# Performance work log

Measured on AMD Instinct MI355X. Metric: run time of the kernel, lower is better.

## Reference

```python
import jax, jax.numpy as jnp
import numpy as np

N, E, G = 200000, 800000, 8000
NODE_IN, EDGE_IN, H = 256, 64, 256


def _mlp2(h, w1, b1, w2, b2):
    return jax.nn.relu(h @ w1 + b1) @ w2 + b2


def setup_inputs() -> dict:
    key = jax.random.key(0)
    ks = jax.random.split(key, 30)
    s = 0.05
    p = lambda k, shp: (jax.random.normal(k, shp, jnp.float32) * s)
    inp = {
        "x": jax.random.normal(ks[0], (N, NODE_IN), jnp.float32),
        "edge_attr": jax.random.normal(ks[1], (E, EDGE_IN), jnp.float32),
        "edge_index": jax.random.randint(ks[2], (2, E), 0, N, dtype=jnp.int32),
        "batch": jnp.sort(jax.random.randint(ks[3], (N,), 0, G, dtype=jnp.int32)),
        # edge MLP
        "em_w1": p(ks[4], (EDGE_IN, H)), "em_b1": jnp.zeros((H,), jnp.float32),
        "em_w2": p(ks[5], (H, H)), "em_b2": jnp.zeros((H,), jnp.float32),
        # GINEConv 1 MLP
        "c1_w1": p(ks[6], (NODE_IN, H)), "c1_b1": jnp.zeros((H,), jnp.float32),
        "c1_w2": p(ks[7], (H, H)), "c1_b2": jnp.zeros((H,), jnp.float32),
        # GINEConv 2 MLP
        "c2_w1": p(ks[8], (H, H)), "c2_b1": jnp.zeros((H,), jnp.float32),
        "c2_w2": p(ks[9], (H, H)), "c2_b2": jnp.zeros((H,), jnp.float32),
        # heads
        "l1_w": p(ks[10], (H, 128)), "l1_b": jnp.zeros((128,), jnp.float32),
        "l2_w": p(ks[11], (128, 64)), "l2_b": jnp.zeros((64,), jnp.float32),
        "hS_w": p(ks[12], (64, 1)), "hS_b": jnp.zeros((1,), jnp.float32),
        "hP_w": p(ks[13], (64, 1)), "hP_b": jnp.zeros((1,), jnp.float32),
        "hN_w": p(ks[14], (64, 1)), "hN_b": jnp.zeros((1,), jnp.float32),
    }
    return inp


def _gine(x, ea, src, dst, w1, b1, w2, b2):
    # GINEConv (eps=0): out = MLP(x_i + sum_j relu(x_j + e_ji))
    msg = jax.nn.relu(x[src] + ea)                      # [E, H]
    agg = jax.ops.segment_sum(msg, dst, num_segments=x.shape[0])
    return _mlp2(x + agg, w1, b1, w2, b2)


def reference(x, edge_attr, edge_index, batch,
              em_w1, em_b1, em_w2, em_b2,
              c1_w1, c1_b1, c1_w2, c1_b2,
              c2_w1, c2_b1, c2_w2, c2_b2,
              l1_w, l1_b, l2_w, l2_b,
              hS_w, hS_b, hP_w, hP_b, hN_w, hN_b):
    src, dst = edge_index[0], edge_index[1]  # source_to_target flow
    ea = _mlp2(edge_attr, em_w1, em_b1, em_w2, em_b2)   # [E, 256]
    h = jax.nn.relu(_gine(x, ea, src, dst, c1_w1, c1_b1, c1_w2, c1_b2))
    h = jax.nn.relu(_gine(h, ea, src, dst, c2_w1, c2_b1, c2_w2, c2_b2))
    # global mean pool over graphs (dropout is identity in eval mode)
    sums = jax.ops.segment_sum(h, batch, num_segments=G)              # [G, 256]
    cnts = jax.ops.segment_sum(jnp.ones((h.shape[0],), h.dtype), batch, num_segments=G)
    pooled = sums / jnp.maximum(cnts, 1.0)[:, None]
    g = jax.nn.relu(pooled @ l1_w + l1_b)
    g = jax.nn.relu(g @ l2_w + l2_b)
    return ((g @ hS_w + hS_b).squeeze(-1),
            (g @ hP_w + hP_b).squeeze(-1),
            (g @ hN_w + hN_b).squeeze(-1))
```

## Files before the change

kernel.cpp:

```cpp
#include <hip/hip_runtime.h>
#include <hip/hip_bf16.h>

typedef __attribute__((ext_vector_type(8))) short short8;
typedef __attribute__((ext_vector_type(4))) float f32x4;
typedef __attribute__((ext_vector_type(2))) unsigned int u32x2;
typedef __attribute__((ext_vector_type(4))) unsigned int u32x4;

#define N_NODES  200000
#define N_EDGES  800000
#define N_GRAPHS 8000

__device__ __forceinline__ unsigned short f2bf(float f) {
  unsigned int u = __float_as_uint(f);
  unsigned int r = (u + 0x7fffu + ((u >> 16) & 1u)) >> 16;
  return (unsigned short)r;
}
__device__ __forceinline__ float bf2f(unsigned short s) {
  return __uint_as_float(((unsigned int)s) << 16);
}
__device__ __forceinline__ unsigned cvtpk(float a, float b) {
  union { __hip_bfloat162 h; unsigned u; } cv;
  cv.h = __float22bfloat162_rn(make_float2(a, b));
  return cv.u;
}

__device__ __forceinline__ void xpose4(unsigned W0, unsigned W1, int bsub,
                                       unsigned selT, unsigned& T0, unsigned& T1) {
  unsigned t0 = (unsigned)__shfl_xor((int)W0, 2);
  unsigned t1 = (unsigned)__shfl_xor((int)W1, 2);
  unsigned A0 = (bsub & 2) ? t1 : W0;
  unsigned A1 = (bsub & 2) ? W1 : t0;
  unsigned t2 = (unsigned)__shfl_xor((int)A0, 1);
  unsigned t3 = (unsigned)__shfl_xor((int)A1, 1);
  T0 = __builtin_amdgcn_perm(A0, t2, selT);
  T1 = __builtin_amdgcn_perm(A1, t3, selT);
}

__global__ void wtrans(const float* __restrict__ w, unsigned short* __restrict__ wt,
                       int K, int Nc) {
  int id = blockIdx.x * 256 + threadIdx.x;
  if (id >= K * Nc) return;
  int k = id / Nc, n = id % Nc;
  wt[n * K + k] = f2bf(w[id]);
}

__global__ __launch_bounds__(256) void x2bf(const float* __restrict__ x,
                                            unsigned short* __restrict__ xb) {
  int id = blockIdx.x * 256 + threadIdx.x;
  if (id >= N_NODES * 256 / 8) return;
  float4 a = ((const float4*)x)[id * 2];
  float4 b = ((const float4*)x)[id * 2 + 1];
  u32x4 pk = {cvtpk(a.x, a.y), cvtpk(a.z, a.w), cvtpk(b.x, b.y), cvtpk(b.z, b.w)};
  ((u32x4*)xb)[id] = pk;
}

template <int K1, int IN_MODE, int SLAB, int NKK>
__device__ __forceinline__ void stage_slab(
    int s, char* ab, int row0, int srow, int skk,
    const float* __restrict__ Xf, const unsigned short* __restrict__ Xb,
    const unsigned short* __restrict__ aggb) {
#pragma unroll
  for (int c2 = 0; c2 < NKK; ++c2) {
    const int kloc = skk + 32 * c2;
    const int gk = s * SLAB + kloc;
    float v[8];
    if (IN_MODE == 0) {
      const float* xp = Xf + (size_t)(row0 + srow) * K1 + gk;
      float4 A = *(const float4*)xp;
      float4 B = *(const float4*)(xp + 4);
      v[0]=A.x; v[1]=A.y; v[2]=A.z; v[3]=A.w; v[4]=B.x; v[5]=B.y; v[6]=B.z; v[7]=B.w;
    } else {
      const unsigned short* hp = Xb + (size_t)(row0 + srow) * 256 + gk;
      short8 hv = *(const short8*)hp;
      const unsigned short* ap = aggb + (size_t)(row0 + srow) * 256 + gk;
      short8 av = *(const short8*)ap;
#pragma unroll
      for (int i = 0; i < 8; ++i)
        v[i] = bf2f((unsigned short)hv[i]) + bf2f((unsigned short)av[i]);
    }
    u32x4 pk;
#pragma unroll
    for (int i = 0; i < 4; ++i) pk[i] = cvtpk(v[2 * i], v[2 * i + 1]);
    int off = srow * (2 * SLAB) + kloc * 2;
    off ^= (srow & 7) << 4;
    *(u32x4*)(ab + off) = pk;
  }
}

template <int K1, int IN_MODE>
__global__ __launch_bounds__(256) void fused_mlp2(
    const float* __restrict__ Xf, const unsigned short* __restrict__ Xb,
    const unsigned short* __restrict__ aggb,
    const unsigned short* __restrict__ w1t, const float* __restrict__ b1,
    const unsigned short* __restrict__ w2t, const float* __restrict__ b2,
    unsigned short* __restrict__ out, int relu_out) {
  constexpr int SLAB  = (K1 < 128) ? K1 : 128;
  constexpr int NSLAB = K1 / SLAB;
  constexpr int NKK   = SLAB / 32;
  __shared__ unsigned short h_lds[64 * 256];
  char* hbase = (char*)h_lds;

  const int tid  = threadIdx.x;
  const int row0 = blockIdx.x * 64;
  const int lane = tid & 63;
  const int wid  = tid >> 6;
  const int lr   = lane & 15;
  const int kq   = lane >> 4;
  const int col0 = wid * 64;
  const int bsub = lr & 3;
  const int asub = lr >> 2;
  const unsigned selT = (bsub & 1) ? 0x07060302u : 0x01000504u;

  const int srow = tid >> 2;
  const int skk  = (tid & 3) * 8;

  f32x4 acc[4][4];
#pragma unroll
  for (int m = 0; m < 4; ++m)
#pragma unroll
    for (int n = 0; n < 4; ++n) acc[m][n] = (f32x4){0.f, 0.f, 0.f, 0.f};

  float bias1[4];
#pragma unroll
  for (int n = 0; n < 4; ++n) bias1[n] = b1[col0 + n * 16 + lr];

  stage_slab<K1, IN_MODE, SLAB, NKK>(0, hbase, row0, srow, skk, Xf, Xb, aggb);
  __syncthreads();

#pragma unroll
  for (int s = 0; s < NSLAB; ++s) {
    if (s + 1 < NSLAB)
      stage_slab<K1, IN_MODE, SLAB, NKK>(s + 1, hbase + 16384, row0, srow, skk,
                                         Xf, Xb, aggb);
    char* ab = hbase + (s & 1) * 16384;
#pragma unroll
    for (int kk = 0; kk < NKK; ++kk) {
      short8 af[4], bq[4];
#pragma unroll
      for (int m = 0; m < 4; ++m) {
        int r = m * 16 + lr;
        int off = r * (2 * SLAB) + kk * 64 + kq * 16;
        off ^= (r & 7) << 4;
        af[m] = *(short8*)(ab + off);
      }
#pragma unroll
      for (int n = 0; n < 4; ++n) {
        int c = col0 + n * 16 + lr;
        bq[n] = *(const short8*)(w1t + (size_t)c * K1 + s * SLAB + kk * 32 + kq * 8);
      }
#pragma unroll
      for (int m = 0; m < 4; ++m)
#pragma unroll
        for (int n = 0; n < 4; ++n)
          acc[m][n] = __builtin_amdgcn_mfma_f32_16x16x32_bf16(af[m], bq[n], acc[m][n], 0, 0, 0);
    }
    __syncthreads();
  }

#pragma unroll
  for (int n = 0; n < 4; ++n) {
    float bn = bias1[n];
#pragma unroll
    for (int m = 0; m < 4; ++m) {
      float v0 = fmaxf(acc[m][n][0] + bn, 0.f);
      float v1 = fmaxf(acc[m][n][1] + bn, 0.f);
      float v2 = fmaxf(acc[m][n][2] + bn, 0.f);
      float v3 = fmaxf(acc[m][n][3] + bn, 0.f);
      unsigned W0 = cvtpk(v0, v1), W1 = cvtpk(v2, v3), T0, T1;
      xpose4(W0, W1, bsub, selT, T0, T1);
      int r = m * 16 + kq * 4 + bsub;
      int cb = col0 + n * 16 + asub * 4;
      int off = r * 512 + cb * 2;
      off ^= (r & 7) << 4;
      *(u32x2*)(hbase + off) = (u32x2){T0, T1};
    }
  }
  __syncthreads();

#pragma unroll
  for (int m = 0; m < 4; ++m)
#pragma unroll
    for (int n = 0; n < 4; ++n) acc[m][n] = (f32x4){0.f, 0.f, 0.f, 0.f};

  float bias2[4];
#pragma unroll
  for (int n = 0; n < 4; ++n) bias2[n] = b2[col0 + n * 16 + lr];

#pragma unroll
  for (int ks = 0; ks < 8; ++ks) {
    short8 af[4], bq[4];
#pragma unroll
    for (int m = 0; m < 4; ++m) {
      int r = m * 16 + lr;
      int off = r * 512 + ks * 64 + kq * 16;
      off ^= (r & 7) << 4;
      af[m] = *(short8*)(hbase + off);
    }
#pragma unroll
    for (int n = 0; n < 4; ++n) {
      int c = col0 + n * 16 + lr;
      bq[n] = *(const short8*)(w2t + (size_t)c * 256 + ks * 32 + kq * 8);
    }
#pragma unroll
    for (int m = 0; m < 4; ++m)
#pragma unroll
      for (int n = 0; n < 4; ++n)
        acc[m][n] = __builtin_amdgcn_mfma_f32_16x16x32_bf16(af[m], bq[n], acc[m][n], 0, 0, 0);
  }
  __syncthreads();

#pragma unroll
  for (int n = 0; n < 4; ++n) {
    float bn = bias2[n];
#pragma unroll
    for (int m = 0; m < 4; ++m) {
      float v0 = acc[m][n][0] + bn;
      float v1 = acc[m][n][1] + bn;
      float v2 = acc[m][n][2] + bn;
      float v3 = acc[m][n][3] + bn;
      if (relu_out) {
        v0 = fmaxf(v0, 0.f); v1 = fmaxf(v1, 0.f);
        v2 = fmaxf(v2, 0.f); v3 = fmaxf(v3, 0.f);
      }
      unsigned W0 = cvtpk(v0, v1), W1 = cvtpk(v2, v3), T0, T1;
      xpose4(W0, W1, bsub, selT, T0, T1);
      int r = m * 16 + kq * 4 + bsub;
      int cb = col0 + n * 16 + asub * 4;
      int off = r * 512 + cb * 2;
      off ^= (r & 7) << 4;
      *(u32x2*)(hbase + off) = (u32x2){T0, T1};
    }
  }
  __syncthreads();

#pragma unroll
  for (int it = 0; it < 8; ++it) {
    int r = (tid >> 5) + it * 8;
    int byte = (tid & 31) * 16;
    int off = (r * 512 + byte) ^ ((r & 7) << 4);
    u32x4 d = *(u32x4*)(hbase + off);
    *(u32x4*)((char*)out + (size_t)(row0 + r) * 512 + byte) = d;
  }
}

__global__ void hist_deg(const int* __restrict__ dst, int* __restrict__ rp) {
  int e = blockIdx.x * 256 + threadIdx.x;
  if (e < N_EDGES) atomicAdd(&rp[dst[e]], 1);
}

__global__ __launch_bounds__(256) void scan_block(int* __restrict__ rp,
                                                  int* __restrict__ bsum) {
  __shared__ int ts[256];
  int b = blockIdx.x, t = threadIdx.x;
  int base = b * 2048 + t * 8;
  int v[8]; int s = 0;
#pragma unroll
  for (int i = 0; i < 8; ++i) {
    int idx = base + i;
    v[i] = (idx < N_NODES) ? rp[idx] : 0;
    s += v[i];
  }
  ts[t] = s;
  __syncthreads();
#pragma unroll
  for (int off = 1; off < 256; off <<= 1) {
    int add = (t >= off) ? ts[t - off] : 0;
    __syncthreads();
    ts[t] += add;
    __syncthreads();
  }
  int excl = ts[t] - s;
  if (t == 255) bsum[b] = ts[255];
  int run = excl;
#pragma unroll
  for (int i = 0; i < 8; ++i) {
    int idx = base + i;
    if (idx < N_NODES) rp[idx] = run;
    run += v[i];
  }
}

__global__ __launch_bounds__(256) void scan_bsum(int* __restrict__ bsum, int nb) {
  __shared__ int ts[256];
  int t = threadIdx.x;
  int v = (t < nb) ? bsum[t] : 0;
  ts[t] = v;
  __syncthreads();
#pragma unroll
  for (int off = 1; off < 256; off <<= 1) {
    int add = (t >= off) ? ts[t - off] : 0;
    __syncthreads();
    ts[t] += add;
    __syncthreads();
  }
  if (t < nb) bsum[t] = ts[t] - v;
}

__global__ void scan_add(int* __restrict__ rp, const int* __restrict__ bsum) {
  int i = blockIdx.x * 256 + threadIdx.x;
  if (i < N_NODES) rp[i] += bsum[i >> 11];
}

__global__ void csr_fill(const int* __restrict__ src, const int* __restrict__ dst,
                         int* __restrict__ rp, int2* __restrict__ csr) {
  int e = blockIdx.x * 256 + threadIdx.x;
  if (e >= N_EDGES) return;
  int d = dst[e];
  int p = atomicAdd(&rp[d], 1);
  csr[p] = make_int2(src[e], e);
}

__global__ __launch_bounds__(256) void gather_agg(
    const unsigned short* __restrict__ ea, const unsigned short* __restrict__ xb,
    const int* __restrict__ rp, const int2* __restrict__ csr,
    unsigned short* __restrict__ agg) {
  int v = blockIdx.x * 4 + (threadIdx.x >> 6);
  if (v >= N_NODES) return;
  int lane = threadIdx.x & 63;
  int c = lane * 4;
  int beg = (v == 0) ? 0 : rp[v - 1];
  int end = rp[v];
  float a0 = 0.f, a1 = 0.f, a2 = 0.f, a3 = 0.f;
  int i = beg;
  for (; i + 2 <= end; i += 2) {
    int2 s0 = csr[i];
    int2 s1 = csr[i + 1];
    ushort4 e0 = *(const ushort4*)(ea + (size_t)s0.y * 256 + c);
    ushort4 e1 = *(const ushort4*)(ea + (size_t)s1.y * 256 + c);
    ushort4 h0 = *(const ushort4*)(xb + (size_t)s0.x * 256 + c);
    ushort4 h1 = *(const ushort4*)(xb + (size_t)s1.x * 256 + c);
    a0 += fmaxf(bf2f(h0.x) + bf2f(e0.x), 0.f) + fmaxf(bf2f(h1.x) + bf2f(e1.x), 0.f);
    a1 += fmaxf(bf2f(h0.y) + bf2f(e0.y), 0.f) + fmaxf(bf2f(h1.y) + bf2f(e1.y), 0.f);
    a2 += fmaxf(bf2f(h0.z) + bf2f(e0.z), 0.f) + fmaxf(bf2f(h1.z) + bf2f(e1.z), 0.f);
    a3 += fmaxf(bf2f(h0.w) + bf2f(e0.w), 0.f) + fmaxf(bf2f(h1.w) + bf2f(e1.w), 0.f);
  }
  if (i < end) {
    int2 se = csr[i];
    ushort4 ev = *(const ushort4*)(ea + (size_t)se.y * 256 + c);
    ushort4 hv = *(const ushort4*)(xb + (size_t)se.x * 256 + c);
    a0 += fmaxf(bf2f(hv.x) + bf2f(ev.x), 0.f);
    a1 += fmaxf(bf2f(hv.y) + bf2f(ev.y), 0.f);
    a2 += fmaxf(bf2f(hv.z) + bf2f(ev.z), 0.f);
    a3 += fmaxf(bf2f(hv.w) + bf2f(ev.w), 0.f);
  }
  u32x2 pk = {cvtpk(a0, a1), cvtpk(a2, a3)};
  *(u32x2*)(agg + (size_t)v * 256 + c) = pk;
}

__global__ __launch_bounds__(256) void pool_mean(const unsigned short* __restrict__ h2,
                                                 const int* __restrict__ batch,
                                                 float* __restrict__ pooled) {
  int g = blockIdx.x;
  int tid = threadIdx.x;
  int lane = tid & 63;
  int sub = tid >> 6;
  int lo = 0, hi = N_NODES;
  while (lo < hi) { int mid = (lo + hi) >> 1; if (batch[mid] < g) lo = mid + 1; else hi = mid; }
  int start = lo;
  hi = N_NODES;
  while (lo < hi) { int mid = (lo + hi) >> 1; if (batch[mid] < g + 1) lo = mid + 1; else hi = mid; }
  int end = lo;
  float s0 = 0.f, s1 = 0.f, s2 = 0.f, s3 = 0.f;
  for (int r = start + sub; r < end; r += 4) {
    ushort4 hv = *(const ushort4*)(h2 + (size_t)r * 256 + lane * 4);
    s0 += bf2f(hv.x); s1 += bf2f(hv.y); s2 += bf2f(hv.z); s3 += bf2f(hv.w);
  }
  __shared__ float4 red[4][64];
  red[sub][lane] = make_float4(s0, s1, s2, s3);
  __syncthreads();
  if (sub == 0) {
    float4 a = red[0][lane], b = red[1][lane], cc = red[2][lane], d = red[3][lane];
    float inv = 1.0f / fmaxf((float)(end - start), 1.0f);
    float4 t = make_float4((a.x + b.x + cc.x + d.x) * inv,
                           (a.y + b.y + cc.y + d.y) * inv,
                           (a.z + b.z + cc.z + d.z) * inv,
                           (a.w + b.w + cc.w + d.w) * inv);
    *(float4*)(pooled + (size_t)g * 256 + lane * 4) = t;
  }
}

__global__ __launch_bounds__(128) void head_mlp(
    const float* __restrict__ pooled, const float* __restrict__ l1w,
    const float* __restrict__ l1b, const float* __restrict__ l2w,
    const float* __restrict__ l2b, const float* __restrict__ hSw,
    const float* __restrict__ hSb, const float* __restrict__ hPw,
    const float* __restrict__ hPb, const float* __restrict__ hNw,
    const float* __restrict__ hNb, float* __restrict__ out) {
  int g = blockIdx.x, tid = threadIdx.x;
  __shared__ float p[256];
  __shared__ float g1[128];
  __shared__ float g2[64];
  p[tid] = pooled[(size_t)g * 256 + tid];
  p[tid + 128] = pooled[(size_t)g * 256 + tid + 128];
  __syncthreads();
  float a = l1b[tid];
#pragma unroll 8
  for (int k = 0; k < 256; ++k) a += p[k] * l1w[k * 128 + tid];
  g1[tid] = fmaxf(a, 0.f);
  __syncthreads();
  if (tid < 64) {
    float b = l2b[tid];
#pragma unroll 8
    for (int k = 0; k < 128; ++k) b += g1[k] * l2w[k * 64 + tid];
    g2[tid] = fmaxf(b, 0.f);
  }
  __syncthreads();
  if (tid < 64) {
    float v = g2[tid];
    float s = v * hSw[tid], pq = v * hPw[tid], nq = v * hNw[tid];
#pragma unroll
    for (int off = 32; off > 0; off >>= 1) {
      s  += __shfl_down(s, off);
      pq += __shfl_down(pq, off);
      nq += __shfl_down(nq, off);
    }
    if (tid == 0) {
      out[g]                = s  + hSb[0];
      out[N_GRAPHS + g]     = pq + hPb[0];
      out[2 * N_GRAPHS + g] = nq + hNb[0];
    }
  }
}

extern "C" void kernel_launch(void* const* d_in, const int* in_sizes, int n_in,
                              void* d_out, int out_size, void* d_ws, size_t ws_size,
                              hipStream_t stream) {
  const float* x         = (const float*)d_in[0];
  const float* edge_attr = (const float*)d_in[1];
  const int*   ei        = (const int*)d_in[2];
  const int*   batch     = (const int*)d_in[3];
  const float* em_w1 = (const float*)d_in[4];  const float* em_b1 = (const float*)d_in[5];
  const float* em_w2 = (const float*)d_in[6];  const float* em_b2 = (const float*)d_in[7];
  const float* c1_w1 = (const float*)d_in[8];  const float* c1_b1 = (const float*)d_in[9];
  const float* c1_w2 = (const float*)d_in[10]; const float* c1_b2 = (const float*)d_in[11];
  const float* c2_w1 = (const float*)d_in[12]; const float* c2_b1 = (const float*)d_in[13];
  const float* c2_w2 = (const float*)d_in[14]; const float* c2_b2 = (const float*)d_in[15];
  const float* l1_w = (const float*)d_in[16];  const float* l1_b = (const float*)d_in[17];
  const float* l2_w = (const float*)d_in[18];  const float* l2_b = (const float*)d_in[19];
  const float* hS_w = (const float*)d_in[20];  const float* hS_b = (const float*)d_in[21];
  const float* hP_w = (const float*)d_in[22];  const float* hP_b = (const float*)d_in[23];
  const float* hN_w = (const float*)d_in[24];  const float* hN_b = (const float*)d_in[25];

  char* ws = (char*)d_ws;
  unsigned short* ea     = (unsigned short*)ws;
  unsigned short* agg    = (unsigned short*)(ws + 409600000);
  unsigned short* xb     = (unsigned short*)(ws + 512000000);
  unsigned short* h1     = (unsigned short*)(ws + 614400000);
  unsigned short* h2     = ea;
  float*          pooled = (float*)(ws + 716800000);
  int2*           csr    = (int2*)(ws + 716800000);
  int*            rp     = (int*)(ws + 723200000);
  int*            bsum   = (int*)(ws + 724000000);
  unsigned short* wt     = (unsigned short*)(ws + 724992000);
  unsigned short* em_w1t = wt;
  unsigned short* em_w2t = em_w1t + 16384;
  unsigned short* c1_w1t = em_w2t + 65536;
  unsigned short* c1_w2t = c1_w1t + 65536;
  unsigned short* c2_w1t = c1_w2t + 65536;
  unsigned short* c2_w2t = c2_w1t + 65536;

  const int* srcI = ei;
  const int* dstI = ei + N_EDGES;

  wtrans<<<(16384 + 255) / 256, 256, 0, stream>>>(em_w1, em_w1t, 64, 256);
  wtrans<<<(65536 + 255) / 256, 256, 0, stream>>>(em_w2, em_w2t, 256, 256);
  wtrans<<<(65536 + 255) / 256, 256, 0, stream>>>(c1_w1, c1_w1t, 256, 256);
  wtrans<<<(65536 + 255) / 256, 256, 0, stream>>>(c1_w2, c1_w2t, 256, 256);
  wtrans<<<(65536 + 255) / 256, 256, 0, stream>>>(c2_w1, c2_w1t, 256, 256);
  wtrans<<<(65536 + 255) / 256, 256, 0, stream>>>(c2_w2, c2_w2t, 256, 256);

  x2bf<<<(N_NODES * 256 / 8 + 255) / 256, 256, 0, stream>>>(x, xb);

  hipMemsetAsync(rp, 0, (size_t)N_NODES * 4, stream);
  hist_deg<<<(N_EDGES + 255) / 256, 256, 0, stream>>>(dstI, rp);
  scan_block<<<(N_NODES + 2047) / 2048, 256, 0, stream>>>(rp, bsum);
  scan_bsum<<<1, 256, 0, stream>>>(bsum, (N_NODES + 2047) / 2048);
  scan_add<<<(N_NODES + 255) / 256, 256, 0, stream>>>(rp, bsum);
  csr_fill<<<N_EDGES / 256, 256, 0, stream>>>(srcI, dstI, rp, csr);

  fused_mlp2<64, 0><<<N_EDGES / 64, 256, 0, stream>>>(
      edge_attr, nullptr, nullptr, em_w1t, em_b1, em_w2t, em_b2, ea, 0);

  gather_agg<<<(N_NODES + 3) / 4, 256, 0, stream>>>(ea, xb, rp, csr, agg);
  fused_mlp2<256, 2><<<N_NODES / 64, 256, 0, stream>>>(
      nullptr, xb, agg, c1_w1t, c1_b1, c1_w2t, c1_b2, h1, 1);

  gather_agg<<<(N_NODES + 3) / 4, 256, 0, stream>>>(ea, h1, rp, csr, agg);
  fused_mlp2<256, 2><<<N_NODES / 64, 256, 0, stream>>>(
      nullptr, h1, agg, c2_w1t, c2_b1, c2_w2t, c2_b2, h2, 1);

  pool_mean<<<N_GRAPHS, 256, 0, stream>>>(h2, batch, pooled);
  head_mlp<<<N_GRAPHS, 128, 0, stream>>>(pooled, l1_w, l1_b, l2_w, l2_b,
                                         hS_w, hS_b, hP_w, hP_b, hN_w, hN_b,
                                         (float*)d_out);
}
```

Measured before the change: 1.181 ms.

## Store edge MLP output in CSR order and load first GEMM operand directly

The edge MLP now writes each edge's embedding at its CSR position through a permutation, so gather_agg reads ea contiguously instead of gathering by edge id, and the CSR array shrinks to source ids only. Separately, the first GEMM of fused_mlp2 drops the LDS double-buffered staging and loads its A fragments straight from global memory into registers. The aim is to cut random-access traffic in the two aggregation passes and remove LDS staging and barriers. The trade-off is scattered row writes in the edge MLP and less coalesced direct A-operand loads with no LDS reuse.

```diff
diff --git a/kernel.cpp b/kernel.cpp
--- a/kernel.cpp
+++ b/kernel.cpp
@@ -54,49 +54,14 @@
   ((u32x4*)xb)[id] = pk;
 }
 
-template <int K1, int IN_MODE, int SLAB, int NKK>
-__device__ __forceinline__ void stage_slab(
-    int s, char* ab, int row0, int srow, int skk,
-    const float* __restrict__ Xf, const unsigned short* __restrict__ Xb,
-    const unsigned short* __restrict__ aggb) {
-#pragma unroll
-  for (int c2 = 0; c2 < NKK; ++c2) {
-    const int kloc = skk + 32 * c2;
-    const int gk = s * SLAB + kloc;
-    float v[8];
-    if (IN_MODE == 0) {
-      const float* xp = Xf + (size_t)(row0 + srow) * K1 + gk;
-      float4 A = *(const float4*)xp;
-      float4 B = *(const float4*)(xp + 4);
-      v[0]=A.x; v[1]=A.y; v[2]=A.z; v[3]=A.w; v[4]=B.x; v[5]=B.y; v[6]=B.z; v[7]=B.w;
-    } else {
-      const unsigned short* hp = Xb + (size_t)(row0 + srow) * 256 + gk;
-      short8 hv = *(const short8*)hp;
-      const unsigned short* ap = aggb + (size_t)(row0 + srow) * 256 + gk;
-      short8 av = *(const short8*)ap;
-#pragma unroll
-      for (int i = 0; i < 8; ++i)
-        v[i] = bf2f((unsigned short)hv[i]) + bf2f((unsigned short)av[i]);
-    }
-    u32x4 pk;
-#pragma unroll
-    for (int i = 0; i < 4; ++i) pk[i] = cvtpk(v[2 * i], v[2 * i + 1]);
-    int off = srow * (2 * SLAB) + kloc * 2;
-    off ^= (srow & 7) << 4;
-    *(u32x4*)(ab + off) = pk;
-  }
-}
-
 template <int K1, int IN_MODE>
 __global__ __launch_bounds__(256) void fused_mlp2(
     const float* __restrict__ Xf, const unsigned short* __restrict__ Xb,
     const unsigned short* __restrict__ aggb,
     const unsigned short* __restrict__ w1t, const float* __restrict__ b1,
     const unsigned short* __restrict__ w2t, const float* __restrict__ b2,
-    unsigned short* __restrict__ out, int relu_out) {
-  constexpr int SLAB  = (K1 < 128) ? K1 : 128;
-  constexpr int NSLAB = K1 / SLAB;
-  constexpr int NKK   = SLAB / 32;
+    unsigned short* __restrict__ out, const int* __restrict__ perm,
+    int relu_out) {
   __shared__ unsigned short h_lds[64 * 256];
   char* hbase = (char*)h_lds;
 
@@ -110,9 +75,7 @@
   const int bsub = lr & 3;
   const int asub = lr >> 2;
   const unsigned selT = (bsub & 1) ? 0x07060302u : 0x01000504u;
-
-  const int srow = tid >> 2;
-  const int skk  = (tid & 3) * 8;
+  const int kbase = kq * 8;
 
   f32x4 acc[4][4];
 #pragma unroll
@@ -124,37 +87,47 @@
 #pragma unroll
   for (int n = 0; n < 4; ++n) bias1[n] = b1[col0 + n * 16 + lr];
 
-  stage_slab<K1, IN_MODE, SLAB, NKK>(0, hbase, row0, srow, skk, Xf, Xb, aggb);
-  __syncthreads();
-
-#pragma unroll
-  for (int s = 0; s < NSLAB; ++s) {
-    if (s + 1 < NSLAB)
-      stage_slab<K1, IN_MODE, SLAB, NKK>(s + 1, hbase + 16384, row0, srow, skk,
-                                         Xf, Xb, aggb);
-    char* ab = hbase + (s & 1) * 16384;
-#pragma unroll
-    for (int kk = 0; kk < NKK; ++kk) {
-      short8 af[4], bq[4];
+#pragma unroll
+  for (int ks = 0; ks < K1 / 32; ++ks) {
+    short8 af[4];
+    if (IN_MODE == 0) {
 #pragma unroll
       for (int m = 0; m < 4; ++m) {
-        int r = m * 16 + lr;
-        int off = r * (2 * SLAB) + kk * 64 + kq * 16;
-        off ^= (r & 7) << 4;
-        af[m] = *(short8*)(ab + off);
+        const float* xp = Xf + (size_t)(row0 + m * 16 + lr) * K1 + ks * 32 + kbase;
+        float4 A = *(const float4*)xp;
+        float4 B = *(const float4*)(xp + 4);
+        u32x4 pk = {cvtpk(A.x, A.y), cvtpk(A.z, A.w), cvtpk(B.x, B.y), cvtpk(B.z, B.w)};
+        af[m] = *(short8*)&pk;
       }
-#pragma unroll
-      for (int n = 0; n < 4; ++n) {
-        int c = col0 + n * 16 + lr;
-        bq[n] = *(const short8*)(w1t + (size_t)c * K1 + s * SLAB + kk * 32 + kq * 8);
+    } else {
+      short8 hv[4], av[4];
+#pragma unroll
+      for (int m = 0; m < 4; ++m) {
+        size_t ro = (size_t)(row0 + m * 16 + lr) * 256 + ks * 32 + kbase;
+        hv[m] = *(const short8*)(Xb + ro);
+        av[m] = *(const short8*)(aggb + ro);
       }
 #pragma unroll
-      for (int m = 0; m < 4; ++m)
-#pragma unroll
-        for (int n = 0; n < 4; ++n)
-          acc[m][n] = __builtin_amdgcn_mfma_f32_16x16x32_bf16(af[m], bq[n], acc[m][n], 0, 0, 0);
-    }
-    __syncthreads();
+      for (int m = 0; m < 4; ++m) {
+        u32x4 pk;
+#pragma unroll
+        for (int i = 0; i < 4; ++i) {
+          float lo = bf2f((unsigned short)hv[m][2 * i])     + bf2f((unsigned short)av[m][2 * i]);
+          float hi = bf2f((unsigned short)hv[m][2 * i + 1]) + bf2f((unsigned short)av[m][2 * i + 1]);
+          pk[i] = cvtpk(lo, hi);
+        }
+        af[m] = *(short8*)&pk;
+      }
+    }
+    short8 bq[4];
+#pragma unroll
+    for (int n = 0; n < 4; ++n)
+      bq[n] = *(const short8*)(w1t + (size_t)(col0 + n * 16 + lr) * K1 + ks * 32 + kbase);
+#pragma unroll
+    for (int m = 0; m < 4; ++m)
+#pragma unroll
+      for (int n = 0; n < 4; ++n)
+        acc[m][n] = __builtin_amdgcn_mfma_f32_16x16x32_bf16(af[m], bq[n], acc[m][n], 0, 0, 0);
   }
 
 #pragma unroll
@@ -239,7 +212,8 @@
     int byte = (tid & 31) * 16;
     int off = (r * 512 + byte) ^ ((r & 7) << 4);
     u32x4 d = *(u32x4*)(hbase + off);
-    *(u32x4*)((char*)out + (size_t)(row0 + r) * 512 + byte) = d;
+    int orow = perm ? perm[row0 + r] : (row0 + r);
+    *(u32x4*)((char*)out + (size_t)orow * 512 + byte) = d;
   }
 }
 
@@ -302,17 +276,18 @@
 }
 
 __global__ void csr_fill(const int* __restrict__ src, const int* __restrict__ dst,
-                         int* __restrict__ rp, int2* __restrict__ csr) {
+                         int* __restrict__ rp, int* __restrict__ csrc,
+                         int* __restrict__ perm) {
   int e = blockIdx.x * 256 + threadIdx.x;
   if (e >= N_EDGES) return;
-  int d = dst[e];
-  int p = atomicAdd(&rp[d], 1);
-  csr[p] = make_int2(src[e], e);
+  int p = atomicAdd(&rp[dst[e]], 1);
+  csrc[p] = src[e];
+  perm[e] = p;
 }
 
 __global__ __launch_bounds__(256) void gather_agg(
     const unsigned short* __restrict__ ea, const unsigned short* __restrict__ xb,
-    const int* __restrict__ rp, const int2* __restrict__ csr,
+    const int* __restrict__ rp, const int* __restrict__ csrc,
     unsigned short* __restrict__ agg) {
   int v = blockIdx.x * 4 + (threadIdx.x >> 6);
   if (v >= N_NODES) return;
@@ -323,21 +298,21 @@
   float a0 = 0.f, a1 = 0.f, a2 = 0.f, a3 = 0.f;
   int i = beg;
   for (; i + 2 <= end; i += 2) {
-    int2 s0 = csr[i];
-    int2 s1 = csr[i + 1];
-    ushort4 e0 = *(const ushort4*)(ea + (size_t)s0.y * 256 + c);
-    ushort4 e1 = *(const ushort4*)(ea + (size_t)s1.y * 256 + c);
-    ushort4 h0 = *(const ushort4*)(xb + (size_t)s0.x * 256 + c);
-    ushort4 h1 = *(const ushort4*)(xb + (size_t)s1.x * 256 + c);
+    int s0 = csrc[i];
+    int s1 = csrc[i + 1];
+    ushort4 e0 = *(const ushort4*)(ea + (size_t)i * 256 + c);
+    ushort4 e1 = *(const ushort4*)(ea + (size_t)(i + 1) * 256 + c);
+    ushort4 h0 = *(const ushort4*)(xb + (size_t)s0 * 256 + c);
+    ushort4 h1 = *(const ushort4*)(xb + (size_t)s1 * 256 + c);
     a0 += fmaxf(bf2f(h0.x) + bf2f(e0.x), 0.f) + fmaxf(bf2f(h1.x) + bf2f(e1.x), 0.f);
     a1 += fmaxf(bf2f(h0.y) + bf2f(e0.y), 0.f) + fmaxf(bf2f(h1.y) + bf2f(e1.y), 0.f);
     a2 += fmaxf(bf2f(h0.z) + bf2f(e0.z), 0.f) + fmaxf(bf2f(h1.z) + bf2f(e1.z), 0.f);
     a3 += fmaxf(bf2f(h0.w) + bf2f(e0.w), 0.f) + fmaxf(bf2f(h1.w) + bf2f(e1.w), 0.f);
   }
   if (i < end) {
-    int2 se = csr[i];
-    ushort4 ev = *(const ushort4*)(ea + (size_t)se.y * 256 + c);
-    ushort4 hv = *(const ushort4*)(xb + (size_t)se.x * 256 + c);
+    int s0 = csrc[i];
+    ushort4 ev = *(const ushort4*)(ea + (size_t)i * 256 + c);
+    ushort4 hv = *(const ushort4*)(xb + (size_t)s0 * 256 + c);
     a0 += fmaxf(bf2f(hv.x) + bf2f(ev.x), 0.f);
     a1 += fmaxf(bf2f(hv.y) + bf2f(ev.y), 0.f);
     a2 += fmaxf(bf2f(hv.z) + bf2f(ev.z), 0.f);
@@ -448,7 +423,8 @@
   unsigned short* h1     = (unsigned short*)(ws + 614400000);
   unsigned short* h2     = ea;
   float*          pooled = (float*)(ws + 716800000);
-  int2*           csr    = (int2*)(ws + 716800000);
+  int*            csrc   = (int*)(ws + 716800000);
+  int*            perm   = (int*)(ws + 720000000);
   int*            rp     = (int*)(ws + 723200000);
   int*            bsum   = (int*)(ws + 724000000);
   unsigned short* wt     = (unsigned short*)(ws + 724992000);
@@ -476,18 +452,18 @@
   scan_block<<<(N_NODES + 2047) / 2048, 256, 0, stream>>>(rp, bsum);
   scan_bsum<<<1, 256, 0, stream>>>(bsum, (N_NODES + 2047) / 2048);
   scan_add<<<(N_NODES + 255) / 256, 256, 0, stream>>>(rp, bsum);
-  csr_fill<<<N_EDGES / 256, 256, 0, stream>>>(srcI, dstI, rp, csr);
+  csr_fill<<<N_EDGES / 256, 256, 0, stream>>>(srcI, dstI, rp, csrc, perm);
 
   fused_mlp2<64, 0><<<N_EDGES / 64, 256, 0, stream>>>(
-      edge_attr, nullptr, nullptr, em_w1t, em_b1, em_w2t, em_b2, ea, 0);
-
-  gather_agg<<<(N_NODES + 3) / 4, 256, 0, stream>>>(ea, xb, rp, csr, agg);
+      edge_attr, nullptr, nullptr, em_w1t, em_b1, em_w2t, em_b2, ea, perm, 0);
+
+  gather_agg<<<(N_NODES + 3) / 4, 256, 0, stream>>>(ea, xb, rp, csrc, agg);
   fused_mlp2<256, 2><<<N_NODES / 64, 256, 0, stream>>>(
-      nullptr, xb, agg, c1_w1t, c1_b1, c1_w2t, c1_b2, h1, 1);
-
-  gather_agg<<<(N_NODES + 3) / 4, 256, 0, stream>>>(ea, h1, rp, csr, agg);
+      nullptr, xb, agg, c1_w1t, c1_b1, c1_w2t, c1_b2, h1, nullptr, 1);
+
+  gather_agg<<<(N_NODES + 3) / 4, 256, 0, stream>>>(ea, h1, rp, csrc, agg);
   fused_mlp2<256, 2><<<N_NODES / 64, 256, 0, stream>>>(
-      nullptr, h1, agg, c2_w1t, c2_b1, c2_w2t, c2_b2, h2, 1);
+      nullptr, h1, agg, c2_w1t, c2_b1, c2_w2t, c2_b2, h2, nullptr, 1);
 
   pool_mean<<<N_GRAPHS, 256, 0, stream>>>(h2, batch, pooled);
   head_mlp<<<N_GRAPHS, 128, 0, stream>>>(pooled, l1_w, l1_b, l2_w, l2_b,
```

Result: slower. 1.417 ms (+20.0%).

## Write edge MLP output in CSR order and pre-convert edge attributes to bf16

Applied to the files above, without the earlier changes.

The edge MLP now scatters each output row to its CSR slot through a permutation array, so gather_agg reads edge embeddings contiguously instead of through the edge id, and the CSR stores only source indices. Edge attributes are converted to bf16 in a separate bulk pass, so the MLP staging is a plain copy. This removes random 512-byte gathers from both aggregation passes at the cost of a scattered write in the edge MLP and an extra conversion kernel. The bf16 edge buffer reuses the h1 region, which is only written after it has been consumed.

```diff
diff --git a/kernel.cpp b/kernel.cpp
--- a/kernel.cpp
+++ b/kernel.cpp
@@ -44,10 +44,11 @@
   wt[n * K + k] = f2bf(w[id]);
 }
 
-__global__ __launch_bounds__(256) void x2bf(const float* __restrict__ x,
-                                            unsigned short* __restrict__ xb) {
+__global__ __launch_bounds__(256) void f2bf_bulk(const float* __restrict__ x,
+                                                 unsigned short* __restrict__ xb,
+                                                 int n8) {
   int id = blockIdx.x * 256 + threadIdx.x;
-  if (id >= N_NODES * 256 / 8) return;
+  if (id >= n8) return;
   float4 a = ((const float4*)x)[id * 2];
   float4 b = ((const float4*)x)[id * 2 + 1];
   u32x4 pk = {cvtpk(a.x, a.y), cvtpk(a.z, a.w), cvtpk(b.x, b.y), cvtpk(b.z, b.w)};
@@ -57,43 +58,42 @@
 template <int K1, int IN_MODE, int SLAB, int NKK>
 __device__ __forceinline__ void stage_slab(
     int s, char* ab, int row0, int srow, int skk,
-    const float* __restrict__ Xf, const unsigned short* __restrict__ Xb,
+    const unsigned short* __restrict__ Xb,
     const unsigned short* __restrict__ aggb) {
 #pragma unroll
   for (int c2 = 0; c2 < NKK; ++c2) {
     const int kloc = skk + 32 * c2;
     const int gk = s * SLAB + kloc;
-    float v[8];
-    if (IN_MODE == 0) {
-      const float* xp = Xf + (size_t)(row0 + srow) * K1 + gk;
-      float4 A = *(const float4*)xp;
-      float4 B = *(const float4*)(xp + 4);
-      v[0]=A.x; v[1]=A.y; v[2]=A.z; v[3]=A.w; v[4]=B.x; v[5]=B.y; v[6]=B.z; v[7]=B.w;
+    int off = srow * (2 * SLAB) + kloc * 2;
+    off ^= (srow & 7) << 4;
+    if (IN_MODE == 3) {
+      u32x4 d = *(const u32x4*)(Xb + (size_t)(row0 + srow) * K1 + gk);
+      *(u32x4*)(ab + off) = d;
     } else {
       const unsigned short* hp = Xb + (size_t)(row0 + srow) * 256 + gk;
       short8 hv = *(const short8*)hp;
       const unsigned short* ap = aggb + (size_t)(row0 + srow) * 256 + gk;
       short8 av = *(const short8*)ap;
+      float v[8];
 #pragma unroll
       for (int i = 0; i < 8; ++i)
         v[i] = bf2f((unsigned short)hv[i]) + bf2f((unsigned short)av[i]);
-    }
-    u32x4 pk;
-#pragma unroll
-    for (int i = 0; i < 4; ++i) pk[i] = cvtpk(v[2 * i], v[2 * i + 1]);
-    int off = srow * (2 * SLAB) + kloc * 2;
-    off ^= (srow & 7) << 4;
-    *(u32x4*)(ab + off) = pk;
+      u32x4 pk;
+#pragma unroll
+      for (int i = 0; i < 4; ++i) pk[i] = cvtpk(v[2 * i], v[2 * i + 1]);
+      *(u32x4*)(ab + off) = pk;
+    }
   }
 }
 
 template <int K1, int IN_MODE>
 __global__ __launch_bounds__(256) void fused_mlp2(
-    const float* __restrict__ Xf, const unsigned short* __restrict__ Xb,
+    const unsigned short* __restrict__ Xb,
     const unsigned short* __restrict__ aggb,
     const unsigned short* __restrict__ w1t, const float* __restrict__ b1,
     const unsigned short* __restrict__ w2t, const float* __restrict__ b2,
-    unsigned short* __restrict__ out, int relu_out) {
+    unsigned short* __restrict__ out, const int* __restrict__ perm,
+    int relu_out) {
   constexpr int SLAB  = (K1 < 128) ? K1 : 128;
   constexpr int NSLAB = K1 / SLAB;
   constexpr int NKK   = SLAB / 32;
@@ -124,14 +124,14 @@
 #pragma unroll
   for (int n = 0; n < 4; ++n) bias1[n] = b1[col0 + n * 16 + lr];
 
-  stage_slab<K1, IN_MODE, SLAB, NKK>(0, hbase, row0, srow, skk, Xf, Xb, aggb);
+  stage_slab<K1, IN_MODE, SLAB, NKK>(0, hbase, row0, srow, skk, Xb, aggb);
   __syncthreads();
 
 #pragma unroll
   for (int s = 0; s < NSLAB; ++s) {
     if (s + 1 < NSLAB)
       stage_slab<K1, IN_MODE, SLAB, NKK>(s + 1, hbase + 16384, row0, srow, skk,
-                                         Xf, Xb, aggb);
+                                         Xb, aggb);
     char* ab = hbase + (s & 1) * 16384;
 #pragma unroll
     for (int kk = 0; kk < NKK; ++kk) {
@@ -239,7 +239,8 @@
     int byte = (tid & 31) * 16;
     int off = (r * 512 + byte) ^ ((r & 7) << 4);
     u32x4 d = *(u32x4*)(hbase + off);
-    *(u32x4*)((char*)out + (size_t)(row0 + r) * 512 + byte) = d;
+    int orow = perm ? perm[row0 + r] : (row0 + r);
+    *(u32x4*)((char*)out + (size_t)orow * 512 + byte) = d;
   }
 }
 
@@ -302,17 +303,18 @@
 }
 
 __global__ void csr_fill(const int* __restrict__ src, const int* __restrict__ dst,
-                         int* __restrict__ rp, int2* __restrict__ csr) {
+                         int* __restrict__ rp, int* __restrict__ csrc,
+                         int* __restrict__ perm) {
   int e = blockIdx.x * 256 + threadIdx.x;
   if (e >= N_EDGES) return;
-  int d = dst[e];
-  int p = atomicAdd(&rp[d], 1);
-  csr[p] = make_int2(src[e], e);
+  int p = atomicAdd(&rp[dst[e]], 1);
+  csrc[p] = src[e];
+  perm[e] = p;
 }
 
 __global__ __launch_bounds__(256) void gather_agg(
     const unsigned short* __restrict__ ea, const unsigned short* __restrict__ xb,
-    const int* __restrict__ rp, const int2* __restrict__ csr,
+    const int* __restrict__ rp, const int* __restrict__ csrc,
     unsigned short* __restrict__ agg) {
   int v = blockIdx.x * 4 + (threadIdx.x >> 6);
   if (v >= N_NODES) return;
@@ -323,21 +325,21 @@
   float a0 = 0.f, a1 = 0.f, a2 = 0.f, a3 = 0.f;
   int i = beg;
   for (; i + 2 <= end; i += 2) {
-    int2 s0 = csr[i];
-    int2 s1 = csr[i + 1];
-    ushort4 e0 = *(const ushort4*)(ea + (size_t)s0.y * 256 + c);
-    ushort4 e1 = *(const ushort4*)(ea + (size_t)s1.y * 256 + c);
-    ushort4 h0 = *(const ushort4*)(xb + (size_t)s0.x * 256 + c);
-    ushort4 h1 = *(const ushort4*)(xb + (size_t)s1.x * 256 + c);
+    int s0 = csrc[i];
+    int s1 = csrc[i + 1];
+    ushort4 e0 = *(const ushort4*)(ea + (size_t)i * 256 + c);
+    ushort4 e1 = *(const ushort4*)(ea + (size_t)(i + 1) * 256 + c);
+    ushort4 h0 = *(const ushort4*)(xb + (size_t)s0 * 256 + c);
+    ushort4 h1 = *(const ushort4*)(xb + (size_t)s1 * 256 + c);
     a0 += fmaxf(bf2f(h0.x) + bf2f(e0.x), 0.f) + fmaxf(bf2f(h1.x) + bf2f(e1.x), 0.f);
     a1 += fmaxf(bf2f(h0.y) + bf2f(e0.y), 0.f) + fmaxf(bf2f(h1.y) + bf2f(e1.y), 0.f);
     a2 += fmaxf(bf2f(h0.z) + bf2f(e0.z), 0.f) + fmaxf(bf2f(h1.z) + bf2f(e1.z), 0.f);
     a3 += fmaxf(bf2f(h0.w) + bf2f(e0.w), 0.f) + fmaxf(bf2f(h1.w) + bf2f(e1.w), 0.f);
   }
   if (i < end) {
-    int2 se = csr[i];
-    ushort4 ev = *(const ushort4*)(ea + (size_t)se.y * 256 + c);
-    ushort4 hv = *(const ushort4*)(xb + (size_t)se.x * 256 + c);
+    int s0 = csrc[i];
+    ushort4 ev = *(const ushort4*)(ea + (size_t)i * 256 + c);
+    ushort4 hv = *(const ushort4*)(xb + (size_t)s0 * 256 + c);
     a0 += fmaxf(bf2f(hv.x) + bf2f(ev.x), 0.f);
     a1 += fmaxf(bf2f(hv.y) + bf2f(ev.y), 0.f);
     a2 += fmaxf(bf2f(hv.z) + bf2f(ev.z), 0.f);
@@ -446,9 +448,11 @@
   unsigned short* agg    = (unsigned short*)(ws + 409600000);
   unsigned short* xb     = (unsigned short*)(ws + 512000000);
   unsigned short* h1     = (unsigned short*)(ws + 614400000);
+  unsigned short* eab    = h1;
   unsigned short* h2     = ea;
   float*          pooled = (float*)(ws + 716800000);
-  int2*           csr    = (int2*)(ws + 716800000);
+  int*            csrc   = (int*)(ws + 716800000);
+  int*            perm   = (int*)(ws + 720000000);
   int*            rp     = (int*)(ws + 723200000);
   int*            bsum   = (int*)(ws + 724000000);
   unsigned short* wt     = (unsigned short*)(ws + 724992000);
@@ -469,25 +473,26 @@
   wtrans<<<(65536 + 255) / 256, 256, 0, stream>>>(c2_w1, c2_w1t, 256, 256);
   wtrans<<<(65536 + 255) / 256, 256, 0, stream>>>(c2_w2, c2_w2t, 256, 256);
 
-  x2bf<<<(N_NODES * 256 / 8 + 255) / 256, 256, 0, stream>>>(x, xb);
+  f2bf_bulk<<<(N_NODES * 256 / 8 + 255) / 256, 256, 0, stream>>>(x, xb, N_NODES * 256 / 8);
+  f2bf_bulk<<<(N_EDGES * 64 / 8 + 255) / 256, 256, 0, stream>>>(edge_attr, eab, N_EDGES * 64 / 8);
 
   hipMemsetAsync(rp, 0, (size_t)N_NODES * 4, stream);
   hist_deg<<<(N_EDGES + 255) / 256, 256, 0, stream>>>(dstI, rp);
   scan_block<<<(N_NODES + 2047) / 2048, 256, 0, stream>>>(rp, bsum);
   scan_bsum<<<1, 256, 0, stream>>>(bsum, (N_NODES + 2047) / 2048);
   scan_add<<<(N_NODES + 255) / 256, 256, 0, stream>>>(rp, bsum);
-  csr_fill<<<N_EDGES / 256, 256, 0, stream>>>(srcI, dstI, rp, csr);
-
-  fused_mlp2<64, 0><<<N_EDGES / 64, 256, 0, stream>>>(
-      edge_attr, nullptr, nullptr, em_w1t, em_b1, em_w2t, em_b2, ea, 0);
-
-  gather_agg<<<(N_NODES + 3) / 4, 256, 0, stream>>>(ea, xb, rp, csr, agg);
+  csr_fill<<<N_EDGES / 256, 256, 0, stream>>>(srcI, dstI, rp, csrc, perm);
+
+  fused_mlp2<64, 3><<<N_EDGES / 64, 256, 0, stream>>>(
+      eab, nullptr, em_w1t, em_b1, em_w2t, em_b2, ea, perm, 0);
+
+  gather_agg<<<(N_NODES + 3) / 4, 256, 0, stream>>>(ea, xb, rp, csrc, agg);
   fused_mlp2<256, 2><<<N_NODES / 64, 256, 0, stream>>>(
-      nullptr, xb, agg, c1_w1t, c1_b1, c1_w2t, c1_b2, h1, 1);
-
-  gather_agg<<<(N_NODES + 3) / 4, 256, 0, stream>>>(ea, h1, rp, csr, agg);
+      xb, agg, c1_w1t, c1_b1, c1_w2t, c1_b2, h1, nullptr, 1);
+
+  gather_agg<<<(N_NODES + 3) / 4, 256, 0, stream>>>(ea, h1, rp, csrc, agg);
   fused_mlp2<256, 2><<<N_NODES / 64, 256, 0, stream>>>(
-      nullptr, h1, agg, c2_w1t, c2_b1, c2_w2t, c2_b2, h2, 1);
+      h1, agg, c2_w1t, c2_b1, c2_w2t, c2_b2, h2, nullptr, 1);
 
   pool_mean<<<N_GRAPHS, 256, 0, stream>>>(h2, batch, pooled);
   head_mlp<<<N_GRAPHS, 128, 0, stream>>>(pooled, l1_w, l1_b, l2_w, l2_b,
```

Result: slower. 1.226 ms (+3.8%).

## Pre-swizzle weights into MFMA fragment order and pre-convert edge attributes to bf16

Applied to the files above, without the earlier changes.

Weight matrices are now stored in per-lane MFMA B-fragment order, so each wavefront's B load becomes one contiguous 1 KB read instead of strided column reads. Edge attributes are converted to bf16 once by a bulk kernel into the free h1 buffer, and the edge MLP stages them straight into LDS without per-element conversion. This adds an extra pass over edge_attr (read fp32, write bf16) in exchange for halving the bytes the edge MLP reads and better-coalesced weight fetches.

```diff
diff --git a/kernel.cpp b/kernel.cpp
--- a/kernel.cpp
+++ b/kernel.cpp
@@ -36,18 +36,26 @@
   T1 = __builtin_amdgcn_perm(A1, t3, selT);
 }
 
-__global__ void wtrans(const float* __restrict__ w, unsigned short* __restrict__ wt,
-                       int K, int Nc) {
+__global__ void wtrans_frag(const float* __restrict__ w, unsigned short* __restrict__ wf,
+                            int K, int Nc) {
   int id = blockIdx.x * 256 + threadIdx.x;
   if (id >= K * Nc) return;
-  int k = id / Nc, n = id % Nc;
-  wt[n * K + k] = f2bf(w[id]);
-}
-
-__global__ __launch_bounds__(256) void x2bf(const float* __restrict__ x,
-                                            unsigned short* __restrict__ xb) {
+  int j    = id & 7;
+  int lane = (id >> 3) & 63;
+  int rest = id >> 9;
+  int KT   = K >> 5;
+  int kt   = rest % KT;
+  int cb   = rest / KT;
+  int c = cb * 16 + (lane & 15);
+  int k = kt * 32 + (lane >> 4) * 8 + j;
+  wf[id] = f2bf(w[k * Nc + c]);
+}
+
+__global__ __launch_bounds__(256) void f2bf_bulk(const float* __restrict__ x,
+                                                 unsigned short* __restrict__ xb,
+                                                 int n8) {
   int id = blockIdx.x * 256 + threadIdx.x;
-  if (id >= N_NODES * 256 / 8) return;
+  if (id >= n8) return;
   float4 a = ((const float4*)x)[id * 2];
   float4 b = ((const float4*)x)[id * 2 + 1];
   u32x4 pk = {cvtpk(a.x, a.y), cvtpk(a.z, a.w), cvtpk(b.x, b.y), cvtpk(b.z, b.w)};
@@ -57,46 +65,45 @@
 template <int K1, int IN_MODE, int SLAB, int NKK>
 __device__ __forceinline__ void stage_slab(
     int s, char* ab, int row0, int srow, int skk,
-    const float* __restrict__ Xf, const unsigned short* __restrict__ Xb,
+    const unsigned short* __restrict__ Xb,
     const unsigned short* __restrict__ aggb) {
 #pragma unroll
   for (int c2 = 0; c2 < NKK; ++c2) {
     const int kloc = skk + 32 * c2;
     const int gk = s * SLAB + kloc;
-    float v[8];
-    if (IN_MODE == 0) {
-      const float* xp = Xf + (size_t)(row0 + srow) * K1 + gk;
-      float4 A = *(const float4*)xp;
-      float4 B = *(const float4*)(xp + 4);
-      v[0]=A.x; v[1]=A.y; v[2]=A.z; v[3]=A.w; v[4]=B.x; v[5]=B.y; v[6]=B.z; v[7]=B.w;
+    int off = srow * (2 * SLAB) + kloc * 2;
+    off ^= (srow & 7) << 4;
+    if (IN_MODE == 3) {
+      u32x4 d = *(const u32x4*)(Xb + (size_t)(row0 + srow) * K1 + gk);
+      *(u32x4*)(ab + off) = d;
     } else {
       const unsigned short* hp = Xb + (size_t)(row0 + srow) * 256 + gk;
       short8 hv = *(const short8*)hp;
       const unsigned short* ap = aggb + (size_t)(row0 + srow) * 256 + gk;
       short8 av = *(const short8*)ap;
+      float v[8];
 #pragma unroll
       for (int i = 0; i < 8; ++i)
         v[i] = bf2f((unsigned short)hv[i]) + bf2f((unsigned short)av[i]);
-    }
-    u32x4 pk;
-#pragma unroll
-    for (int i = 0; i < 4; ++i) pk[i] = cvtpk(v[2 * i], v[2 * i + 1]);
-    int off = srow * (2 * SLAB) + kloc * 2;
-    off ^= (srow & 7) << 4;
-    *(u32x4*)(ab + off) = pk;
+      u32x4 pk;
+#pragma unroll
+      for (int i = 0; i < 4; ++i) pk[i] = cvtpk(v[2 * i], v[2 * i + 1]);
+      *(u32x4*)(ab + off) = pk;
+    }
   }
 }
 
 template <int K1, int IN_MODE>
 __global__ __launch_bounds__(256) void fused_mlp2(
-    const float* __restrict__ Xf, const unsigned short* __restrict__ Xb,
+    const unsigned short* __restrict__ Xb,
     const unsigned short* __restrict__ aggb,
-    const unsigned short* __restrict__ w1t, const float* __restrict__ b1,
-    const unsigned short* __restrict__ w2t, const float* __restrict__ b2,
+    const unsigned short* __restrict__ w1f, const float* __restrict__ b1,
+    const unsigned short* __restrict__ w2f, const float* __restrict__ b2,
     unsigned short* __restrict__ out, int relu_out) {
   constexpr int SLAB  = (K1 < 128) ? K1 : 128;
   constexpr int NSLAB = K1 / SLAB;
   constexpr int NKK   = SLAB / 32;
+  constexpr int KT1   = K1 / 32;
   __shared__ unsigned short h_lds[64 * 256];
   char* hbase = (char*)h_lds;
 
@@ -107,6 +114,7 @@
   const int lr   = lane & 15;
   const int kq   = lane >> 4;
   const int col0 = wid * 64;
+  const int cb0  = wid * 4;
   const int bsub = lr & 3;
   const int asub = lr >> 2;
   const unsigned selT = (bsub & 1) ? 0x07060302u : 0x01000504u;
@@ -124,14 +132,14 @@
 #pragma unroll
   for (int n = 0; n < 4; ++n) bias1[n] = b1[col0 + n * 16 + lr];
 
-  stage_slab<K1, IN_MODE, SLAB, NKK>(0, hbase, row0, srow, skk, Xf, Xb, aggb);
+  stage_slab<K1, IN_MODE, SLAB, NKK>(0, hbase, row0, srow, skk, Xb, aggb);
   __syncthreads();
 
 #pragma unroll
   for (int s = 0; s < NSLAB; ++s) {
     if (s + 1 < NSLAB)
       stage_slab<K1, IN_MODE, SLAB, NKK>(s + 1, hbase + 16384, row0, srow, skk,
-                                         Xf, Xb, aggb);
+                                         Xb, aggb);
     char* ab = hbase + (s & 1) * 16384;
 #pragma unroll
     for (int kk = 0; kk < NKK; ++kk) {
@@ -143,11 +151,10 @@
         off ^= (r & 7) << 4;
         af[m] = *(short8*)(ab + off);
       }
-#pragma unroll
-      for (int n = 0; n < 4; ++n) {
-        int c = col0 + n * 16 + lr;
-        bq[n] = *(const short8*)(w1t + (size_t)c * K1 + s * SLAB + kk * 32 + kq * 8);
-      }
+      const int kt = s * NKK + kk;
+#pragma unroll
+      for (int n = 0; n < 4; ++n)
+        bq[n] = *(const short8*)(w1f + ((size_t)(cb0 + n) * KT1 + kt) * 512 + lane * 8);
 #pragma unroll
       for (int m = 0; m < 4; ++m)
 #pragma unroll
@@ -197,10 +204,8 @@
       af[m] = *(short8*)(hbase + off);
     }
 #pragma unroll
-    for (int n = 0; n < 4; ++n) {
-      int c = col0 + n * 16 + lr;
-      bq[n] = *(const short8*)(w2t + (size_t)c * 256 + ks * 32 + kq * 8);
-    }
+    for (int n = 0; n < 4; ++n)
+      bq[n] = *(const short8*)(w2f + ((size_t)(cb0 + n) * 8 + ks) * 512 + lane * 8);
 #pragma unroll
     for (int m = 0; m < 4; ++m)
 #pragma unroll
@@ -446,30 +451,32 @@
   unsigned short* agg    = (unsigned short*)(ws + 409600000);
   unsigned short* xb     = (unsigned short*)(ws + 512000000);
   unsigned short* h1     = (unsigned short*)(ws + 614400000);
+  unsigned short* eab    = h1;
   unsigned short* h2     = ea;
   float*          pooled = (float*)(ws + 716800000);
   int2*           csr    = (int2*)(ws + 716800000);
   int*            rp     = (int*)(ws + 723200000);
   int*            bsum   = (int*)(ws + 724000000);
   unsigned short* wt     = (unsigned short*)(ws + 724992000);
-  unsigned short* em_w1t = wt;
-  unsigned short* em_w2t = em_w1t + 16384;
-  unsigned short* c1_w1t = em_w2t + 65536;
-  unsigned short* c1_w2t = c1_w1t + 65536;
-  unsigned short* c2_w1t = c1_w2t + 65536;
-  unsigned short* c2_w2t = c2_w1t + 65536;
+  unsigned short* em_w1f = wt;
+  unsigned short* em_w2f = em_w1f + 16384;
+  unsigned short* c1_w1f = em_w2f + 65536;
+  unsigned short* c1_w2f = c1_w1f + 65536;
+  unsigned short* c2_w1f = c1_w2f + 65536;
+  unsigned short* c2_w2f = c2_w1f + 65536;
 
   const int* srcI = ei;
   const int* dstI = ei + N_EDGES;
 
-  wtrans<<<(16384 + 255) / 256, 256, 0, stream>>>(em_w1, em_w1t, 64, 256);
-  wtrans<<<(65536 + 255) / 256, 256, 0, stream>>>(em_w2, em_w2t, 256, 256);
-  wtrans<<<(65536 + 255) / 256, 256, 0, stream>>>(c1_w1, c1_w1t, 256, 256);
-  wtrans<<<(65536 + 255) / 256, 256, 0, stream>>>(c1_w2, c1_w2t, 256, 256);
-  wtrans<<<(65536 + 255) / 256, 256, 0, stream>>>(c2_w1, c2_w1t, 256, 256);
-  wtrans<<<(65536 + 255) / 256, 256, 0, stream>>>(c2_w2, c2_w2t, 256, 256);
-
-  x2bf<<<(N_NODES * 256 / 8 + 255) / 256, 256, 0, stream>>>(x, xb);
+  wtrans_frag<<<(16384 + 255) / 256, 256, 0, stream>>>(em_w1, em_w1f, 64, 256);
+  wtrans_frag<<<(65536 + 255) / 256, 256, 0, stream>>>(em_w2, em_w2f, 256, 256);
+  wtrans_frag<<<(65536 + 255) / 256, 256, 0, stream>>>(c1_w1, c1_w1f, 256, 256);
+  wtrans_frag<<<(65536 + 255) / 256, 256, 0, stream>>>(c1_w2, c1_w2f, 256, 256);
+  wtrans_frag<<<(65536 + 255) / 256, 256, 0, stream>>>(c2_w1, c2_w1f, 256, 256);
+  wtrans_frag<<<(65536 + 255) / 256, 256, 0, stream>>>(c2_w2, c2_w2f, 256, 256);
+
+  f2bf_bulk<<<(N_NODES * 256 / 8 + 255) / 256, 256, 0, stream>>>(x, xb, N_NODES * 256 / 8);
+  f2bf_bulk<<<(N_EDGES * 64 / 8 + 255) / 256, 256, 0, stream>>>(edge_attr, eab, N_EDGES * 64 / 8);
 
   hipMemsetAsync(rp, 0, (size_t)N_NODES * 4, stream);
   hist_deg<<<(N_EDGES + 255) / 256, 256, 0, stream>>>(dstI, rp);
@@ -478,16 +485,16 @@
   scan_add<<<(N_NODES + 255) / 256, 256, 0, stream>>>(rp, bsum);
   csr_fill<<<N_EDGES / 256, 256, 0, stream>>>(srcI, dstI, rp, csr);
 
-  fused_mlp2<64, 0><<<N_EDGES / 64, 256, 0, stream>>>(
-      edge_attr, nullptr, nullptr, em_w1t, em_b1, em_w2t, em_b2, ea, 0);
+  fused_mlp2<64, 3><<<N_EDGES / 64, 256, 0, stream>>>(
+      eab, nullptr, em_w1f, em_b1, em_w2f, em_b2, ea, 0);
 
   gather_agg<<<(N_NODES + 3) / 4, 256, 0, stream>>>(ea, xb, rp, csr, agg);
   fused_mlp2<256, 2><<<N_NODES / 64, 256, 0, stream>>>(
-      nullptr, xb, agg, c1_w1t, c1_b1, c1_w2t, c1_b2, h1, 1);
+      xb, agg, c1_w1f, c1_b1, c1_w2f, c1_b2, h1, 1);
 
   gather_agg<<<(N_NODES + 3) / 4, 256, 0, stream>>>(ea, h1, rp, csr, agg);
   fused_mlp2<256, 2><<<N_NODES / 64, 256, 0, stream>>>(
-      nullptr, h1, agg, c2_w1t, c2_b1, c2_w2t, c2_b2, h2, 1);
+      h1, agg, c2_w1f, c2_b1, c2_w2f, c2_b2, h2, 1);
 
   pool_mean<<<N_GRAPHS, 256, 0, stream>>>(h2, batch, pooled);
   head_mlp<<<N_GRAPHS, 128, 0, stream>>>(pooled, l1_w, l1_b, l2_w, l2_b,
```

New measurement: 1.048 ms. -11.3%, faster.
